# Performance work log

Measured on AMD Instinct MI355X. Metric: run time of the kernel, lower is better.

The kernel has to match this reference:

```python
import jax, jax.numpy as jnp
import numpy as np

DIM = 192
WIN = 7
HEADS = 6
N = WIN * WIN
B_ = 8192
NW = 1024  # windows per image; B_ // NW images


def _relative_position_index(win):
    coords = np.stack(np.meshgrid(np.arange(win), np.arange(win), indexing='ij'))  # [2,Wh,Ww]
    flat = coords.reshape(2, -1)  # [2,N]
    rel = flat[:, :, None] - flat[:, None, :]  # [2,N,N]
    rel = rel.transpose(1, 2, 0)
    rel[..., 0] += win - 1
    rel[..., 1] += win - 1
    rel[..., 0] *= 2 * win - 1
    return jnp.asarray(rel[..., 0] + rel[..., 1], dtype=jnp.int32)  # [N,N]


def setup_inputs() -> dict:
    key = jax.random.key(0)
    ks = jax.random.split(key, 7)
    x = jax.random.normal(ks[0], (B_, WIN, WIN, DIM), dtype=jnp.float32)
    mask = jnp.zeros((NW, N, N), dtype=jnp.float32)
    qkv_w = jax.random.normal(ks[1], (3 * DIM, DIM), dtype=jnp.float32) * 0.02
    qkv_b = jnp.zeros((3 * DIM,), dtype=jnp.float32)
    proj_w = jax.random.normal(ks[2], (DIM, DIM), dtype=jnp.float32) * 0.02
    proj_b = jnp.zeros((DIM,), dtype=jnp.float32)
    num_rel = (2 * WIN - 1) * (2 * WIN - 1)
    rel_bias_table = jax.random.truncated_normal(ks[3], -2.0, 2.0, (num_rel, HEADS), dtype=jnp.float32) * 0.02
    rel_index = _relative_position_index(WIN)
    return {"x": x, "mask": mask, "qkv_w": qkv_w, "qkv_b": qkv_b,
            "proj_w": proj_w, "proj_b": proj_b,
            "rel_bias_table": rel_bias_table, "rel_index": rel_index}


def reference(x, mask, qkv_w, qkv_b, proj_w, proj_b, rel_bias_table, rel_index):
    Bw, Wh, Ww, C = x.shape
    n = Wh * Ww
    H = HEADS
    hd = C // H
    scale = hd ** -0.5
    xf = x.reshape(Bw, n, C)
    qkv = xf @ qkv_w.T + qkv_b  # [Bw, n, 3C]
    qkv = qkv.reshape(Bw, n, 3, H, hd).transpose(2, 0, 3, 1, 4)  # [3, Bw, H, n, hd]
    q, k, v = qkv[0], qkv[1], qkv[2]
    attn = jnp.einsum('bhnd,bhmd->bhnm', q * scale, k)  # [Bw, H, n, n]
    bias = rel_bias_table[rel_index.reshape(-1)].reshape(n, n, H).transpose(2, 0, 1)  # [H,n,n]
    attn = attn + bias[None]
    nw = mask.shape[0]
    attn = attn.reshape(Bw // nw, nw, H, n, n) + mask[None, :, None]
    attn = attn.reshape(Bw, H, n, n)
    attn = jax.nn.softmax(attn, axis=-1)
    out = jnp.einsum('bhnm,bhmd->bhnd', attn, v)  # [Bw,H,n,hd]
    out = out.transpose(0, 2, 1, 3).reshape(Bw, n, C)
    return out @ proj_w.T + proj_b
```

## Files before the change

### kernel.cpp

```cpp
#include <hip/hip_runtime.h>
#include <hip/hip_bf16.h>

#define NSEQ 49
#define DIMC 192
#define NHEAD 6
#define HD 32
#define NWIN 1024
#define NBLK 8192
#define QSCALE 0.17677669529663687f

typedef __bf16 bf16x8 __attribute__((ext_vector_type(8)));
typedef float f32x4 __attribute__((ext_vector_type(4)));
typedef unsigned short ushort4v __attribute__((ext_vector_type(4)));

#define WQ_OFF 0
#define WP_OFF 221184
#define BIAS_OFF 294912
#define QB_OFF 352544
#define PB_OFF 354848

__device__ __forceinline__ unsigned short f2bf(float f) {
  unsigned int u = __builtin_bit_cast(unsigned int, f);
  u += 0x7fffu + ((u >> 16) & 1u);
  return (unsigned short)(u >> 16);
}

__device__ __forceinline__ f32x4 mfma16(bf16x8 a, bf16x8 b, f32x4 c) {
  return __builtin_amdgcn_mfma_f32_16x16x32_bf16(a, b, c, 0, 0, 0);
}

__global__ void prep_kernel(const float* __restrict__ qkv_w, const float* __restrict__ qkv_b,
                            const float* __restrict__ proj_w, const float* __restrict__ proj_b,
                            const float* __restrict__ table, const int* __restrict__ ridx,
                            char* __restrict__ ws) {
  unsigned short* wq = (unsigned short*)(ws + WQ_OFF);
  unsigned short* wp = (unsigned short*)(ws + WP_OFF);
  float* biasf = (float*)(ws + BIAS_OFF);
  float* qb = (float*)(ws + QB_OFF);
  float* pb = (float*)(ws + PB_OFF);
  int idx = blockIdx.x * blockDim.x + threadIdx.x;
  const int T0 = 576*192, T1 = T0 + 192*192, T2 = T1 + NHEAD*NSEQ*NSEQ, T3 = T2 + 576, T4 = T3 + 192;
  if (idx < T0) {
    float f = qkv_w[idx];
    if (idx < 192*192) f *= QSCALE;
    wq[idx] = f2bf(f);
  } else if (idx < T1) {
    int i = idx - T0;
    wp[i] = f2bf(proj_w[i]);
  } else if (idx < T2) {
    int i = idx - T1;
    int h = i / (NSEQ*NSEQ), rc = i - h*(NSEQ*NSEQ);
    biasf[i] = table[ridx[rc]*NHEAD + h];
  } else if (idx < T3) {
    int i = idx - T2;
    qb[i] = qkv_b[i] * (i < 192 ? QSCALE : 1.0f);
  } else if (idx < T4) {
    int i = idx - T3;
    pb[i] = proj_b[i];
  }
}

__global__ __launch_bounds__(512)
void wattn_kernel(const float* __restrict__ x, const float* __restrict__ mask,
                  const char* __restrict__ ws, float* __restrict__ out) {
  __shared__ __align__(16) char smem[130816];
  unsigned short* xs = (unsigned short*)smem;
  float* S = (float*)smem;
  unsigned short* P  = (unsigned short*)(smem + 16896);
  unsigned short* qs = (unsigned short*)(smem + 26112);
  unsigned short* ks = (unsigned short*)(smem + 51712);
  unsigned short* vs = (unsigned short*)(smem + 77312);
  unsigned short* os = (unsigned short*)(smem + 104960);
  float* rsum = (float*)(smem + 130560);

  const unsigned short* wq = (const unsigned short*)(ws + WQ_OFF);
  const unsigned short* wp = (const unsigned short*)(ws + WP_OFF);
  const float* biasf = (const float*)(ws + BIAS_OFF);
  const float* qb = (const float*)(ws + QB_OFF);
  const float* pb = (const float*)(ws + PB_OFF);

  const int tid = threadIdx.x;
  const int wave = tid >> 6, lane = tid & 63;
  const int lhi = lane >> 4, llo = lane & 15;
  const int win = blockIdx.x;

  {
    const float* xp = x + (size_t)win * (NSEQ*DIMC);
    for (int idx = tid; idx < 64*48; idx += 512) {
      int r = idx / 48, c4 = idx - r*48;
      float4 f = make_float4(0.f, 0.f, 0.f, 0.f);
      if (r < NSEQ) f = *(const float4*)(xp + r*DIMC + c4*4);
      ushort4v u = { f2bf(f.x), f2bf(f.y), f2bf(f.z), f2bf(f.w) };
      *(ushort4v*)(xs + r*200 + c4*4) = u;
    }
  }
  __syncthreads();

  for (int s = wave; s < 36; s += 8) {
    const unsigned short* wrow = wq + (s*16 + llo)*DIMC + lhi*8;
    bf16x8 b0 = *(const bf16x8*)(wrow +   0);
    bf16x8 b1 = *(const bf16x8*)(wrow +  32);
    bf16x8 b2 = *(const bf16x8*)(wrow +  64);
    bf16x8 b3 = *(const bf16x8*)(wrow +  96);
    bf16x8 b4 = *(const bf16x8*)(wrow + 128);
    bf16x8 b5 = *(const bf16x8*)(wrow + 160);
    f32x4 acc[4];
    #pragma unroll
    for (int rt = 0; rt < 4; ++rt) {
      const unsigned short* ar = xs + (rt*16 + llo)*200 + lhi*8;
      f32x4 a = {0.f, 0.f, 0.f, 0.f};
      a = mfma16(*(const bf16x8*)(ar +   0), b0, a);
      a = mfma16(*(const bf16x8*)(ar +  32), b1, a);
      a = mfma16(*(const bf16x8*)(ar +  64), b2, a);
      a = mfma16(*(const bf16x8*)(ar +  96), b3, a);
      a = mfma16(*(const bf16x8*)(ar + 128), b4, a);
      a = mfma16(*(const bf16x8*)(ar + 160), b5, a);
      acc[rt] = a;
    }
    float bn = qb[s*16 + llo];
    #pragma unroll
    for (int rt = 0; rt < 4; ++rt) {
      #pragma unroll
      for (int i = 0; i < 4; ++i) {
        int row = rt*16 + lhi*4 + i;
        unsigned short hv = f2bf(acc[rt][i] + bn);
        if (s < 12)      qs[row*200 + s*16 + llo] = hv;
        else if (s < 24) ks[row*200 + (s-12)*16 + llo] = hv;
        else             vs[((s-24)*16 + llo)*72 + row] = hv;
      }
    }
  }
  __syncthreads();

  const float* mrow = mask + (size_t)(win & (NWIN-1)) * (NSEQ*NSEQ);
  for (int h = 0; h < NHEAD; ++h) {
    #pragma unroll
    for (int tt = 0; tt < 2; ++tt) {
      int t = wave*2 + tt;
      int ti = t >> 2, tj = t & 3;
      bf16x8 a = *(const bf16x8*)(qs + (ti*16 + llo)*200 + h*HD + lhi*8);
      bf16x8 b = *(const bf16x8*)(ks + (tj*16 + llo)*200 + h*HD + lhi*8);
      f32x4 acc = {0.f, 0.f, 0.f, 0.f};
      acc = mfma16(a, b, acc);
      int col = tj*16 + llo;
      const float* brow = biasf + h*(NSEQ*NSEQ);
      #pragma unroll
      for (int i = 0; i < 4; ++i) {
        int row = ti*16 + lhi*4 + i;
        float v;
        if (col < NSEQ) {
          v = acc[i];
          if (row < NSEQ) v += brow[row*NSEQ + col] + mrow[row*NSEQ + col];
        } else {
          v = -1e30f;
        }
        S[row*66 + col] = v;
      }
    }
    __syncthreads();
    {
      int r = tid >> 3, sub = tid & 7;
      float* Sr = S + r*66;
      unsigned short* Pr = P + r*72;
      if (r < NSEQ) {
        float vals[8];
        float m = -1e30f;
        #pragma unroll
        for (int t = 0; t < 8; ++t) { vals[t] = Sr[sub + 8*t]; m = fmaxf(m, vals[t]); }
        m = fmaxf(m, __shfl_xor(m, 1));
        m = fmaxf(m, __shfl_xor(m, 2));
        m = fmaxf(m, __shfl_xor(m, 4));
        float sum = 0.f;
        #pragma unroll
        for (int t = 0; t < 8; ++t) {
          float e = __expf(vals[t] - m);
          sum += e;
          Pr[sub + 8*t] = f2bf(e);
        }
        sum += __shfl_xor(sum, 1);
        sum += __shfl_xor(sum, 2);
        sum += __shfl_xor(sum, 4);
        if (sub == 0) rsum[r] = 1.f / sum;
      } else {
        #pragma unroll
        for (int t = 0; t < 8; ++t) Pr[sub + 8*t] = 0;
        if (sub == 0) rsum[r] = 0.f;
      }
    }
    __syncthreads();
    {
      int rt = wave >> 1, ct = wave & 1;
      f32x4 acc = {0.f, 0.f, 0.f, 0.f};
      #pragma unroll
      for (int kk = 0; kk < 2; ++kk) {
        bf16x8 a = *(const bf16x8*)(P  + (rt*16 + llo)*72 + kk*32 + lhi*8);
        bf16x8 b = *(const bf16x8*)(vs + (h*HD + ct*16 + llo)*72 + kk*32 + lhi*8);
        acc = mfma16(a, b, acc);
      }
      #pragma unroll
      for (int i = 0; i < 4; ++i) {
        int row = rt*16 + lhi*4 + i;
        os[row*200 + h*HD + ct*16 + llo] = f2bf(acc[i] * rsum[row]);
      }
    }
    __syncthreads();
  }

  for (int s = wave; s < 12; s += 8) {
    const unsigned short* wrow = wp + (s*16 + llo)*DIMC + lhi*8;
    bf16x8 b0 = *(const bf16x8*)(wrow +   0);
    bf16x8 b1 = *(const bf16x8*)(wrow +  32);
    bf16x8 b2 = *(const bf16x8*)(wrow +  64);
    bf16x8 b3 = *(const bf16x8*)(wrow +  96);
    bf16x8 b4 = *(const bf16x8*)(wrow + 128);
    bf16x8 b5 = *(const bf16x8*)(wrow + 160);
    f32x4 acc[4];
    #pragma unroll
    for (int rt = 0; rt < 4; ++rt) {
      const unsigned short* ar = os + (rt*16 + llo)*200 + lhi*8;
      f32x4 a = {0.f, 0.f, 0.f, 0.f};
      a = mfma16(*(const bf16x8*)(ar +   0), b0, a);
      a = mfma16(*(const bf16x8*)(ar +  32), b1, a);
      a = mfma16(*(const bf16x8*)(ar +  64), b2, a);
      a = mfma16(*(const bf16x8*)(ar +  96), b3, a);
      a = mfma16(*(const bf16x8*)(ar + 128), b4, a);
      a = mfma16(*(const bf16x8*)(ar + 160), b5, a);
      acc[rt] = a;
    }
    float pbn = pb[s*16 + llo];
    #pragma unroll
    for (int rt = 0; rt < 4; ++rt) {
      #pragma unroll
      for (int i = 0; i < 4; ++i) {
        int row = rt*16 + lhi*4 + i;
        if (row < NSEQ)
          out[((size_t)win*NSEQ + row)*DIMC + s*16 + llo] = acc[rt][i] + pbn;
      }
    }
  }
}

extern "C" void kernel_launch(void* const* d_in, const int* in_sizes, int n_in,
                              void* d_out, int out_size, void* d_ws, size_t ws_size,
                              hipStream_t stream) {
  const float* x      = (const float*)d_in[0];
  const float* mask   = (const float*)d_in[1];
  const float* qkv_w  = (const float*)d_in[2];
  const float* qkv_b  = (const float*)d_in[3];
  const float* proj_w = (const float*)d_in[4];
  const float* proj_b = (const float*)d_in[5];
  const float* table  = (const float*)d_in[6];
  const int*   ridx   = (const int*)d_in[7];
  float* out = (float*)d_out;
  char* ws = (char*)d_ws;

  const int prep_total = 576*192 + 192*192 + NHEAD*NSEQ*NSEQ + 576 + 192;
  prep_kernel<<<(prep_total + 255)/256, 256, 0, stream>>>(qkv_w, qkv_b, proj_w, proj_b, table, ridx, ws);
  wattn_kernel<<<NBLK, 512, 0, stream>>>(x, mask, ws, out);
}
```

Measured before the change: 1.315 ms.

## Restructure window attention to one wave per head with register-resident softmax

Drops to 6 waves, one per head, and keeps the score tile, softmax and P in registers, using lane shuffles to re-layout P for the PV MFMA. This removes the per-head shared-memory round trips and the three barriers per head. X is loaded straight from global into register MFMA fragments, and shared memory is cut to 72KB with XOR-swizzled layouts so two blocks can share a CU. The cost is higher register pressure under launch_bounds(384,2) and a more intricate shuffle-based data layout.

```diff
diff --git a/kernel.cpp b/kernel.cpp
--- a/kernel.cpp
+++ b/kernel.cpp
@@ -4,14 +4,15 @@
 #define NSEQ 49
 #define DIMC 192
 #define NHEAD 6
-#define HD 32
 #define NWIN 1024
 #define NBLK 8192
+#define NN 2401
 #define QSCALE 0.17677669529663687f
 
 typedef __bf16 bf16x8 __attribute__((ext_vector_type(8)));
 typedef float f32x4 __attribute__((ext_vector_type(4)));
-typedef unsigned short ushort4v __attribute__((ext_vector_type(4)));
+typedef unsigned int u32x4 __attribute__((ext_vector_type(4)));
+typedef unsigned short u16;
 
 #define WQ_OFF 0
 #define WP_OFF 221184
@@ -19,27 +20,37 @@
 #define QB_OFF 352544
 #define PB_OFF 354848
 
-__device__ __forceinline__ unsigned short f2bf(float f) {
+__device__ __forceinline__ u16 f2bf(float f) {
   unsigned int u = __builtin_bit_cast(unsigned int, f);
   u += 0x7fffu + ((u >> 16) & 1u);
-  return (unsigned short)(u >> 16);
-}
-
+  return (u16)(u >> 16);
+}
 __device__ __forceinline__ f32x4 mfma16(bf16x8 a, bf16x8 b, f32x4 c) {
   return __builtin_amdgcn_mfma_f32_16x16x32_bf16(a, b, c, 0, 0, 0);
+}
+__device__ __forceinline__ f32x4 ld4u(const float* p) {
+  f32x4 v; __builtin_memcpy(&v, p, 16); return v;
+}
+__device__ __forceinline__ bf16x8 pack8(f32x4 a, f32x4 b) {
+  u32x4 w;
+  w[0] = f2bf(a[0]) | ((unsigned)f2bf(a[1]) << 16);
+  w[1] = f2bf(a[2]) | ((unsigned)f2bf(a[3]) << 16);
+  w[2] = f2bf(b[0]) | ((unsigned)f2bf(b[1]) << 16);
+  w[3] = f2bf(b[2]) | ((unsigned)f2bf(b[3]) << 16);
+  return __builtin_bit_cast(bf16x8, w);
 }
 
 __global__ void prep_kernel(const float* __restrict__ qkv_w, const float* __restrict__ qkv_b,
                             const float* __restrict__ proj_w, const float* __restrict__ proj_b,
                             const float* __restrict__ table, const int* __restrict__ ridx,
                             char* __restrict__ ws) {
-  unsigned short* wq = (unsigned short*)(ws + WQ_OFF);
-  unsigned short* wp = (unsigned short*)(ws + WP_OFF);
+  u16* wq = (u16*)(ws + WQ_OFF);
+  u16* wp = (u16*)(ws + WP_OFF);
   float* biasf = (float*)(ws + BIAS_OFF);
   float* qb = (float*)(ws + QB_OFF);
   float* pb = (float*)(ws + PB_OFF);
   int idx = blockIdx.x * blockDim.x + threadIdx.x;
-  const int T0 = 576*192, T1 = T0 + 192*192, T2 = T1 + NHEAD*NSEQ*NSEQ, T3 = T2 + 576, T4 = T3 + 192;
+  const int T0 = 576*192, T1 = T0 + 192*192, T2 = T1 + NHEAD*NN, T3 = T2 + 576, T4 = T3 + 192;
   if (idx < T0) {
     float f = qkv_w[idx];
     if (idx < 192*192) f *= QSCALE;
@@ -49,7 +60,7 @@
     wp[i] = f2bf(proj_w[i]);
   } else if (idx < T2) {
     int i = idx - T1;
-    int h = i / (NSEQ*NSEQ), rc = i - h*(NSEQ*NSEQ);
+    int h = i / NN, rc = i - h*NN;
     biasf[i] = table[ridx[rc]*NHEAD + h];
   } else if (idx < T3) {
     int i = idx - T2;
@@ -60,181 +71,219 @@
   }
 }
 
-__global__ __launch_bounds__(512)
+__global__ __launch_bounds__(384, 2)
 void wattn_kernel(const float* __restrict__ x, const float* __restrict__ mask,
                   const char* __restrict__ ws, float* __restrict__ out) {
-  __shared__ __align__(16) char smem[130816];
-  unsigned short* xs = (unsigned short*)smem;
-  float* S = (float*)smem;
-  unsigned short* P  = (unsigned short*)(smem + 16896);
-  unsigned short* qs = (unsigned short*)(smem + 26112);
-  unsigned short* ks = (unsigned short*)(smem + 51712);
-  unsigned short* vs = (unsigned short*)(smem + 77312);
-  unsigned short* os = (unsigned short*)(smem + 104960);
-  float* rsum = (float*)(smem + 130560);
-
-  const unsigned short* wq = (const unsigned short*)(ws + WQ_OFF);
-  const unsigned short* wp = (const unsigned short*)(ws + WP_OFF);
+  __shared__ __align__(16) char smem[73728];
+  char* qkb = smem;
+  char* vsb = smem + 49152;
+
+  const u16* wq = (const u16*)(ws + WQ_OFF);
+  const u16* wp = (const u16*)(ws + WP_OFF);
   const float* biasf = (const float*)(ws + BIAS_OFF);
   const float* qb = (const float*)(ws + QB_OFF);
   const float* pb = (const float*)(ws + PB_OFF);
 
   const int tid = threadIdx.x;
-  const int wave = tid >> 6, lane = tid & 63;
+  const int wave = tid >> 6;
+  const int lane = tid & 63;
   const int lhi = lane >> 4, llo = lane & 15;
   const int win = blockIdx.x;
-
+  const int h = wave;
+
+  bf16x8 xa[4][6];
   {
     const float* xp = x + (size_t)win * (NSEQ*DIMC);
-    for (int idx = tid; idx < 64*48; idx += 512) {
-      int r = idx / 48, c4 = idx - r*48;
-      float4 f = make_float4(0.f, 0.f, 0.f, 0.f);
-      if (r < NSEQ) f = *(const float4*)(xp + r*DIMC + c4*4);
-      ushort4v u = { f2bf(f.x), f2bf(f.y), f2bf(f.z), f2bf(f.w) };
-      *(ushort4v*)(xs + r*200 + c4*4) = u;
-    }
-  }
-  __syncthreads();
-
-  for (int s = wave; s < 36; s += 8) {
-    const unsigned short* wrow = wq + (s*16 + llo)*DIMC + lhi*8;
+    #pragma unroll
+    for (int rt = 0; rt < 4; ++rt) {
+      int row = rt*16 + llo;
+      bool valid = (row < NSEQ);
+      const float* pr = xp + row*DIMC + lhi*8;
+      #pragma unroll
+      for (int kk = 0; kk < 6; ++kk) {
+        f32x4 f0 = {0.f,0.f,0.f,0.f}, f1 = {0.f,0.f,0.f,0.f};
+        if (valid) { f0 = *(const f32x4*)(pr + kk*32); f1 = *(const f32x4*)(pr + kk*32 + 4); }
+        xa[rt][kk] = pack8(f0, f1);
+      }
+    }
+  }
+
+  #pragma unroll
+  for (int cc = 0; cc < 6; ++cc) {
+    int s = (cc < 2) ? (wave*2 + cc)
+          : (cc < 4) ? (12 + wave*2 + (cc - 2))
+                     : (24 + wave*2 + (cc - 4));
+    const u16* wrow = wq + (s*16 + llo)*DIMC + lhi*8;
     bf16x8 b0 = *(const bf16x8*)(wrow +   0);
     bf16x8 b1 = *(const bf16x8*)(wrow +  32);
     bf16x8 b2 = *(const bf16x8*)(wrow +  64);
     bf16x8 b3 = *(const bf16x8*)(wrow +  96);
     bf16x8 b4 = *(const bf16x8*)(wrow + 128);
     bf16x8 b5 = *(const bf16x8*)(wrow + 160);
-    f32x4 acc[4];
+    float bn = qb[s*16 + llo];
     #pragma unroll
     for (int rt = 0; rt < 4; ++rt) {
-      const unsigned short* ar = xs + (rt*16 + llo)*200 + lhi*8;
-      f32x4 a = {0.f, 0.f, 0.f, 0.f};
-      a = mfma16(*(const bf16x8*)(ar +   0), b0, a);
-      a = mfma16(*(const bf16x8*)(ar +  32), b1, a);
-      a = mfma16(*(const bf16x8*)(ar +  64), b2, a);
-      a = mfma16(*(const bf16x8*)(ar +  96), b3, a);
-      a = mfma16(*(const bf16x8*)(ar + 128), b4, a);
-      a = mfma16(*(const bf16x8*)(ar + 160), b5, a);
-      acc[rt] = a;
-    }
-    float bn = qb[s*16 + llo];
-    #pragma unroll
-    for (int rt = 0; rt < 4; ++rt) {
+      f32x4 acc = {0.f,0.f,0.f,0.f};
+      acc = mfma16(xa[rt][0], b0, acc);
+      acc = mfma16(xa[rt][1], b1, acc);
+      acc = mfma16(xa[rt][2], b2, acc);
+      acc = mfma16(xa[rt][3], b3, acc);
+      acc = mfma16(xa[rt][4], b4, acc);
+      acc = mfma16(xa[rt][5], b5, acc);
+      if (cc < 4) {
+        int col = s*16 + llo;
+        #pragma unroll
+        for (int i = 0; i < 4; ++i) {
+          int row = rt*16 + lhi*4 + i;
+          *(u16*)(qkb + row*768 + ((col*2) ^ ((row&7)<<4))) = f2bf(acc[i] + bn);
+        }
+      } else {
+        int d = (s - 24)*16 + llo;
+        #pragma unroll
+        for (int i = 0; i < 4; ++i) {
+          int seq = rt*16 + lhi*4 + i;
+          *(u16*)(vsb + d*128 + ((seq*2) ^ ((d&7)<<4))) = f2bf(acc[i] + bn);
+        }
+      }
+    }
+  }
+
+  __syncthreads();
+
+  bf16x8 kf[4], qf[4];
+  #pragma unroll
+  for (int tt = 0; tt < 4; ++tt) {
+    int row = tt*16 + llo;
+    kf[tt] = *(const bf16x8*)(qkb + row*768 + ((((192 + h*32)*2) + lhi*16) ^ ((row&7)<<4)));
+    qf[tt] = *(const bf16x8*)(qkb + row*768 + ((((h*32)*2) + lhi*16) ^ ((row&7)<<4)));
+  }
+  f32x4 t[4][4];
+  #pragma unroll
+  for (int kt = 0; kt < 4; ++kt)
+    #pragma unroll
+    for (int qt = 0; qt < 4; ++qt) {
+      f32x4 z = {0.f,0.f,0.f,0.f};
+      t[kt][qt] = mfma16(kf[kt], qf[qt], z);
+    }
+
+  {
+    const float* brow = biasf + h*NN;
+    const float* mrow = mask + (size_t)(win & (NWIN-1))*NN;
+    #pragma unroll
+    for (int qt = 0; qt < 4; ++qt) {
+      int q = qt*16 + llo;
+      if (q < NSEQ) {
+        #pragma unroll
+        for (int kt = 0; kt < 3; ++kt) {
+          int kb = kt*16 + lhi*4;
+          f32x4 b4 = ld4u(brow + q*NSEQ + kb);
+          f32x4 m4 = ld4u(mrow + q*NSEQ + kb);
+          #pragma unroll
+          for (int i = 0; i < 4; ++i) t[kt][qt][i] += b4[i] + m4[i];
+        }
+        if (lhi == 0) t[3][qt][0] += brow[q*NSEQ + 48] + mrow[q*NSEQ + 48];
+      }
+    }
+  }
+
+  unsigned int pk[4][4][2];
+  #pragma unroll
+  for (int qt = 0; qt < 4; ++qt) {
+    float m = -1e30f;
+    #pragma unroll
+    for (int kt = 0; kt < 3; ++kt)
+      #pragma unroll
+      for (int i = 0; i < 4; ++i) m = fmaxf(m, t[kt][qt][i]);
+    if (lhi == 0) m = fmaxf(m, t[3][qt][0]);
+    m = fmaxf(m, __shfl_xor(m, 16));
+    m = fmaxf(m, __shfl_xor(m, 32));
+    float sum = 0.f;
+    #pragma unroll
+    for (int kt = 0; kt < 3; ++kt)
+      #pragma unroll
+      for (int i = 0; i < 4; ++i) { float e = __expf(t[kt][qt][i] - m); t[kt][qt][i] = e; sum += e; }
+    { float e = (lhi == 0) ? __expf(t[3][qt][0] - m) : 0.f; t[3][qt][0] = e; sum += e; }
+    t[3][qt][1] = 0.f; t[3][qt][2] = 0.f; t[3][qt][3] = 0.f;
+    sum += __shfl_xor(sum, 16);
+    sum += __shfl_xor(sum, 32);
+    float inv = 1.f / sum;
+    #pragma unroll
+    for (int kt = 0; kt < 4; ++kt) {
+      float p0 = t[kt][qt][0]*inv, p1 = t[kt][qt][1]*inv;
+      float p2 = t[kt][qt][2]*inv, p3 = t[kt][qt][3]*inv;
+      pk[kt][qt][0] = f2bf(p0) | ((unsigned)f2bf(p1) << 16);
+      pk[kt][qt][1] = f2bf(p2) | ((unsigned)f2bf(p3) << 16);
+    }
+  }
+
+  f32x4 o[4][2];
+  #pragma unroll
+  for (int qt = 0; qt < 4; ++qt)
+    #pragma unroll
+    for (int dt = 0; dt < 2; ++dt) o[qt][dt] = (f32x4){0.f,0.f,0.f,0.f};
+  #pragma unroll
+  for (int kk = 0; kk < 2; ++kk) {
+    bf16x8 pa[4];
+    #pragma unroll
+    for (int qt = 0; qt < 4; ++qt) {
+      u32x4 w;
+      #pragma unroll
+      for (int ee = 0; ee < 4; ++ee) {
+        int src = (((lhi & 1)*2 + (ee >> 1)) << 4) + llo;
+        int wA = __shfl((int)pk[2*kk    ][qt][ee & 1], src);
+        int wB = __shfl((int)pk[2*kk + 1][qt][ee & 1], src);
+        w[ee] = (lhi < 2) ? (unsigned)wA : (unsigned)wB;
+      }
+      pa[qt] = __builtin_bit_cast(bf16x8, w);
+    }
+    #pragma unroll
+    for (int dt = 0; dt < 2; ++dt) {
+      int dg = h*32 + dt*16 + llo;
+      bf16x8 vf = *(const bf16x8*)(vsb + dg*128 + ((kk*64 + lhi*16) ^ ((dg&7)<<4)));
+      #pragma unroll
+      for (int qt = 0; qt < 4; ++qt) o[qt][dt] = mfma16(pa[qt], vf, o[qt][dt]);
+    }
+  }
+
+  #pragma unroll
+  for (int qt = 0; qt < 4; ++qt)
+    #pragma unroll
+    for (int dt = 0; dt < 2; ++dt)
       #pragma unroll
       for (int i = 0; i < 4; ++i) {
-        int row = rt*16 + lhi*4 + i;
-        unsigned short hv = f2bf(acc[rt][i] + bn);
-        if (s < 12)      qs[row*200 + s*16 + llo] = hv;
-        else if (s < 24) ks[row*200 + (s-12)*16 + llo] = hv;
-        else             vs[((s-24)*16 + llo)*72 + row] = hv;
-      }
-    }
-  }
+        int row = qt*16 + lhi*4 + i;
+        int col = h*32 + dt*16 + llo;
+        *(u16*)(qkb + row*768 + ((col*2) ^ ((row&7)<<4))) = f2bf(o[qt][dt][i]);
+      }
+
   __syncthreads();
 
-  const float* mrow = mask + (size_t)(win & (NWIN-1)) * (NSEQ*NSEQ);
-  for (int h = 0; h < NHEAD; ++h) {
-    #pragma unroll
-    for (int tt = 0; tt < 2; ++tt) {
-      int t = wave*2 + tt;
-      int ti = t >> 2, tj = t & 3;
-      bf16x8 a = *(const bf16x8*)(qs + (ti*16 + llo)*200 + h*HD + lhi*8);
-      bf16x8 b = *(const bf16x8*)(ks + (tj*16 + llo)*200 + h*HD + lhi*8);
-      f32x4 acc = {0.f, 0.f, 0.f, 0.f};
-      acc = mfma16(a, b, acc);
-      int col = tj*16 + llo;
-      const float* brow = biasf + h*(NSEQ*NSEQ);
-      #pragma unroll
-      for (int i = 0; i < 4; ++i) {
-        int row = ti*16 + lhi*4 + i;
-        float v;
-        if (col < NSEQ) {
-          v = acc[i];
-          if (row < NSEQ) v += brow[row*NSEQ + col] + mrow[row*NSEQ + col];
-        } else {
-          v = -1e30f;
-        }
-        S[row*66 + col] = v;
-      }
-    }
-    __syncthreads();
-    {
-      int r = tid >> 3, sub = tid & 7;
-      float* Sr = S + r*66;
-      unsigned short* Pr = P + r*72;
-      if (r < NSEQ) {
-        float vals[8];
-        float m = -1e30f;
-        #pragma unroll
-        for (int t = 0; t < 8; ++t) { vals[t] = Sr[sub + 8*t]; m = fmaxf(m, vals[t]); }
-        m = fmaxf(m, __shfl_xor(m, 1));
-        m = fmaxf(m, __shfl_xor(m, 2));
-        m = fmaxf(m, __shfl_xor(m, 4));
-        float sum = 0.f;
-        #pragma unroll
-        for (int t = 0; t < 8; ++t) {
-          float e = __expf(vals[t] - m);
-          sum += e;
-          Pr[sub + 8*t] = f2bf(e);
-        }
-        sum += __shfl_xor(sum, 1);
-        sum += __shfl_xor(sum, 2);
-        sum += __shfl_xor(sum, 4);
-        if (sub == 0) rsum[r] = 1.f / sum;
-      } else {
-        #pragma unroll
-        for (int t = 0; t < 8; ++t) Pr[sub + 8*t] = 0;
-        if (sub == 0) rsum[r] = 0.f;
-      }
-    }
-    __syncthreads();
-    {
-      int rt = wave >> 1, ct = wave & 1;
-      f32x4 acc = {0.f, 0.f, 0.f, 0.f};
-      #pragma unroll
-      for (int kk = 0; kk < 2; ++kk) {
-        bf16x8 a = *(const bf16x8*)(P  + (rt*16 + llo)*72 + kk*32 + lhi*8);
-        bf16x8 b = *(const bf16x8*)(vs + (h*HD + ct*16 + llo)*72 + kk*32 + lhi*8);
-        acc = mfma16(a, b, acc);
-      }
-      #pragma unroll
-      for (int i = 0; i < 4; ++i) {
-        int row = rt*16 + lhi*4 + i;
-        os[row*200 + h*HD + ct*16 + llo] = f2bf(acc[i] * rsum[row]);
-      }
-    }
-    __syncthreads();
-  }
-
-  for (int s = wave; s < 12; s += 8) {
-    const unsigned short* wrow = wp + (s*16 + llo)*DIMC + lhi*8;
+  #pragma unroll
+  for (int ss = 0; ss < 2; ++ss) {
+    int s = wave + ss*6;
+    const u16* wrow = wp + (s*16 + llo)*DIMC + lhi*8;
     bf16x8 b0 = *(const bf16x8*)(wrow +   0);
     bf16x8 b1 = *(const bf16x8*)(wrow +  32);
     bf16x8 b2 = *(const bf16x8*)(wrow +  64);
     bf16x8 b3 = *(const bf16x8*)(wrow +  96);
     bf16x8 b4 = *(const bf16x8*)(wrow + 128);
     bf16x8 b5 = *(const bf16x8*)(wrow + 160);
-    f32x4 acc[4];
+    float bn = pb[s*16 + llo];
     #pragma unroll
     for (int rt = 0; rt < 4; ++rt) {
-      const unsigned short* ar = os + (rt*16 + llo)*200 + lhi*8;
-      f32x4 a = {0.f, 0.f, 0.f, 0.f};
-      a = mfma16(*(const bf16x8*)(ar +   0), b0, a);
-      a = mfma16(*(const bf16x8*)(ar +  32), b1, a);
-      a = mfma16(*(const bf16x8*)(ar +  64), b2, a);
-      a = mfma16(*(const bf16x8*)(ar +  96), b3, a);
-      a = mfma16(*(const bf16x8*)(ar + 128), b4, a);
-      a = mfma16(*(const bf16x8*)(ar + 160), b5, a);
-      acc[rt] = a;
-    }
-    float pbn = pb[s*16 + llo];
-    #pragma unroll
-    for (int rt = 0; rt < 4; ++rt) {
+      int arow = rt*16 + llo;
+      f32x4 acc = {0.f,0.f,0.f,0.f};
+      acc = mfma16(*(const bf16x8*)(qkb + arow*768 + ((  0 + lhi*16) ^ ((arow&7)<<4))), b0, acc);
+      acc = mfma16(*(const bf16x8*)(qkb + arow*768 + (( 64 + lhi*16) ^ ((arow&7)<<4))), b1, acc);
+      acc = mfma16(*(const bf16x8*)(qkb + arow*768 + ((128 + lhi*16) ^ ((arow&7)<<4))), b2, acc);
+      acc = mfma16(*(const bf16x8*)(qkb + arow*768 + ((192 + lhi*16) ^ ((arow&7)<<4))), b3, acc);
+      acc = mfma16(*(const bf16x8*)(qkb + arow*768 + ((256 + lhi*16) ^ ((arow&7)<<4))), b4, acc);
+      acc = mfma16(*(const bf16x8*)(qkb + arow*768 + ((320 + lhi*16) ^ ((arow&7)<<4))), b5, acc);
       #pragma unroll
       for (int i = 0; i < 4; ++i) {
         int row = rt*16 + lhi*4 + i;
         if (row < NSEQ)
-          out[((size_t)win*NSEQ + row)*DIMC + s*16 + llo] = acc[rt][i] + pbn;
+          out[((size_t)win*NSEQ + row)*DIMC + s*16 + llo] = acc[i] + bn;
       }
     }
   }
@@ -254,7 +303,7 @@
   float* out = (float*)d_out;
   char* ws = (char*)d_ws;
 
-  const int prep_total = 576*192 + 192*192 + NHEAD*NSEQ*NSEQ + 576 + 192;
+  const int prep_total = 576*192 + 192*192 + NHEAD*NN + 576 + 192;
   prep_kernel<<<(prep_total + 255)/256, 256, 0, stream>>>(qkv_w, qkv_b, proj_w, proj_b, table, ridx, ws);
-  wattn_kernel<<<NBLK, 512, 0, stream>>>(x, mask, ws, out);
-}
+  wattn_kernel<<<NBLK, 384, 0, stream>>>(x, mask, ws, out);
+}
```

After: 1.103 ms. 16.1% less time.
